# Performance work log

Hardware: AMD Instinct MI355X
Metric: run time of the kernel (lower is better)

The kernel has to match this reference:

```python
import jax, jax.numpy as jnp
import numpy as np

TP, M, K, N_GLOBAL = 8, 4096, 8192, 8192
K_LOCAL = K // TP      # 1024
N_LOCAL = N_GLOBAL // TP  # 1024


def setup_inputs() -> dict:
    key = jax.random.key(0)
    k1, k2, k3 = jax.random.split(key, 3)
    # all_act[r] is rank r's local activation shard (M, K_local);
    # the fused kernel all-gathers these into the gathered buffer.
    all_act = jax.random.normal(k1, (TP, M, K_LOCAL), dtype=jnp.float32)
    # local_W: this rank's weight shard, full K rows, N_local columns.
    local_W = jax.random.normal(k2, (K, N_LOCAL), dtype=jnp.float32) / np.sqrt(K)
    bias = jax.random.normal(k3, (N_LOCAL,), dtype=jnp.float32)
    return {"all_act": all_act, "local_W": local_W, "bias": bias}


def reference(all_act, local_W, bias):
    # Kernel accumulates, per source rank r:
    #   acc += A_shard[r] (M, K_local) @ W[r*K_local:(r+1)*K_local] (K_local, N_local)
    # which equals A_full @ W_local with A_full the K-concat of shards.
    W_shards = local_W.reshape(TP, K_LOCAL, N_LOCAL)
    out = jnp.einsum('rmk,rkn->mn', all_act, W_shards)  # (M, N_local)
    return out + bias[None, :]
```

## Files before the change

kernel.cpp:

```cpp
#include <hip/hip_runtime.h>
#include <stdint.h>

#define TP_      8
#define M_DIM    4096
#define K_DIM    8192
#define N_DIM    1024
#define KL_      1024
#define BM       256
#define BN       256
#define SPLITK   4
#define KSLICE   (K_DIM / SPLITK)
#define MN4      (M_DIM * N_DIM / 4)
#define KCHUNKS  (K_DIM / 32)
#define NBLK_A   ((M_DIM / 16) * (K_DIM / 32) / 4)
#define NBLK_W   ((N_DIM / 64) * (K_DIM / 64))

typedef _Float16 f16;
typedef f16 f16x8 __attribute__((ext_vector_type(8)));
typedef f16 f16x4 __attribute__((ext_vector_type(4)));
typedef float f32x4 __attribute__((ext_vector_type(4)));

__device__ __forceinline__ f16x8 cvt8(float4 a, float4 b) {
    f16x8 r;
    r[0] = (f16)a.x; r[1] = (f16)a.y; r[2] = (f16)a.z; r[3] = (f16)a.w;
    r[4] = (f16)b.x; r[5] = (f16)b.y; r[6] = (f16)b.z; r[7] = (f16)b.w;
    return r;
}

__device__ __forceinline__ void lds_load16(const void* g, void* l) {
    __builtin_amdgcn_global_load_lds(
        (const __attribute__((address_space(1))) void*)g,
        (__attribute__((address_space(3))) void*)l, 16, 0, 0);
}


__global__ __launch_bounds__(256) void conv_aw_kernel(
        const float* __restrict__ act, const float* __restrict__ W,
        f16* __restrict__ Afrag, f16* __restrict__ Bfrag) {
    __shared__ float tile[64][68];
    const int bid = blockIdx.x;
    const int t   = threadIdx.x;
    if (bid < NBLK_A) {
        const int chunkId = bid * 4 + (t >> 6);
        const int lane = t & 63;
        const int q  = lane >> 4;
        const int rr = lane & 15;
        const int mg  = chunkId >> 8;
        const int k32 = chunkId & 255;
        const int k  = k32 * 32 + q * 8;
        const int r  = k >> 10;
        const int kl = k & (KL_ - 1);
        const int m  = mg * 16 + rr;
        const float4* src = (const float4*)(act + ((size_t)r * M_DIM + m) * KL_ + kl);
        float4 a = src[0], b = src[1];
        *(f16x8*)(Afrag + (size_t)chunkId * 512 + lane * 8) = cvt8(a, b);
        return;
    }
    const int b2 = bid - NBLK_A;
    const int n0 = (b2 & 15) * 64;
    const int k0 = (b2 >> 4) * 64;
    #pragma unroll
    for (int l = 0; l < 4; l++) {
        int kr = l * 16 + (t >> 4);
        float4 v = *(const float4*)&W[(size_t)(k0 + kr) * N_DIM + n0 + (t & 15) * 4];
        *(float4*)&tile[kr][(t & 15) * 4] = v;
    }
    __syncthreads();
    const int jtl   = t >> 6;
    const int kt32l = (t >> 5) & 1;
    const int u     = t & 31;
    const int rr    = u & 15;
    const int qp    = u >> 4;
    f16x8 h0, h1;
    #pragma unroll
    for (int kk = 0; kk < 8; kk++)
        h0[kk] = (f16)tile[kt32l * 32 + qp * 16 + kk][jtl * 16 + rr];
    #pragma unroll
    for (int kk = 0; kk < 8; kk++)
        h1[kk] = (f16)tile[kt32l * 32 + qp * 16 + 8 + kk][jtl * 16 + rr];
    size_t chunk = (size_t)(n0 / 16 + jtl) * KCHUNKS + (k0 / 32 + kt32l);
    f16* dst = Bfrag + chunk * 512;
    *(f16x8*)(dst + ((2 * qp)     * 16 + rr) * 8) = h0;
    *(f16x8*)(dst + ((2 * qp + 1) * 16 + rr) * 8) = h1;
}

__global__ __launch_bounds__(512, 2) void gemm_frag_kernel(
        const f16* __restrict__ Afrag,
        const f16* __restrict__ Bfrag,
        f16* __restrict__ part) {
    __shared__ f16 sm[2][64 * 512];

    const int tid  = threadIdx.x;
    const int w    = tid >> 6;
    const int lane = tid & 63;
    const int q    = lane >> 4;
    const int rr   = lane & 15;
    const int wr   = w >> 2;
    const int wc   = w & 3;

    const int id   = blockIdx.x;
    const int xcd  = id & 7;
    const int slot = id >> 3;
    const int z    = xcd >> 1;
    const int mb   = (slot >> 2) * 2 + (xcd & 1);
    const int nb   = slot & 3;
    const int row0 = mb * BM;
    const int col0 = nb * BN;
    const int kb32 = z * (KSLICE / 32);
    const int mg0  = row0 >> 4;
    const int ng0  = col0 >> 4;

    f32x4 acc[8][4];
    #pragma unroll
    for (int m = 0; m < 8; m++)
        #pragma unroll
        for (int n = 0; n < 4; n++)
            acc[m][n] = (f32x4){0.f, 0.f, 0.f, 0.f};

    f16x8 af[8];
    f16x8 bf[2];

#define STAGE_A(B_, T_, K2_) do { \
    const int kt32_ = kb32 + 2 * (T_) + (K2_); \
    _Pragma("unroll") \
    for (int j_ = 0; j_ < 2; j_++) { \
        const int mg_ = 2 * w + j_; \
        const f16* g_ = Afrag + ((size_t)(mg0 + mg_) * KCHUNKS + kt32_) * 512 + lane * 8; \
        lds_load16(g_, &sm[B_][(mg_ * 2 + (K2_)) * 512 + lane * 8]); \
    } \
} while (0)

#define STAGE_B(B_, T_, K2_) do { \
    const int kt32_ = kb32 + 2 * (T_) + (K2_); \
    _Pragma("unroll") \
    for (int j_ = 0; j_ < 2; j_++) { \
        const int ng_ = 2 * w + j_; \
        const f16* g_ = Bfrag + ((size_t)(ng0 + ng_) * KCHUNKS + kt32_) * 512 + lane * 8; \
        lds_load16(g_, &sm[B_][(32 + ng_ * 2 + (K2_)) * 512 + lane * 8]); \
    } \
} while (0)

#define READ_A(B_, K2_) do { \
    _Pragma("unroll") \
    for (int mi_ = 0; mi_ < 8; mi_++) \
        af[mi_] = *(const f16x8*)&sm[B_][((wr * 8 + mi_) * 2 + (K2_)) * 512 + lane * 8]; \
} while (0)

#define READ_B(B_, K2_, NH_) do { \
    _Pragma("unroll") \
    for (int ni_ = 0; ni_ < 2; ni_++) \
        bf[ni_] = *(const f16x8*)&sm[B_][(32 + (wc * 4 + (NH_) * 2 + ni_) * 2 + (K2_)) * 512 + lane * 8]; \
} while (0)

#define MFMA16(NH_) do { \
    __builtin_amdgcn_s_setprio(1); \
    _Pragma("unroll") \
    for (int mi_ = 0; mi_ < 8; mi_++) \
        _Pragma("unroll") \
        for (int ni_ = 0; ni_ < 2; ni_++) \
            acc[mi_][(NH_) * 2 + ni_] = __builtin_amdgcn_mfma_f32_16x16x32_f16( \
                af[mi_], bf[ni_], acc[mi_][(NH_) * 2 + ni_], 0, 0, 0); \
    __builtin_amdgcn_s_setprio(0); \
} while (0)

#define BAR() do { \
    asm volatile("" ::: "memory"); \
    __builtin_amdgcn_s_barrier(); \
    asm volatile("" ::: "memory"); \
} while (0)
#define SBAR0() __builtin_amdgcn_sched_barrier(0)
#define VM4() asm volatile("s_waitcnt vmcnt(4)" ::: "memory")
#define VM0() asm volatile("s_waitcnt vmcnt(0)" ::: "memory")

#define TILE(P_, T_, STG_, VMMID_, VMEND_) do { \
    READ_A(P_, 0); READ_B(P_, 0, 0); \
    if (STG_) STAGE_A((P_) ^ 1, (T_) + 1, 0); \
    BAR(); SBAR0(); MFMA16(0); BAR(); \
    READ_B(P_, 0, 1); \
    if (STG_) STAGE_B((P_) ^ 1, (T_) + 1, 0); \
    BAR(); SBAR0(); MFMA16(1); VMMID_; BAR(); \
    READ_A(P_, 1); READ_B(P_, 1, 0); \
    if (STG_) STAGE_A((P_) ^ 1, (T_) + 1, 1); \
    BAR(); SBAR0(); MFMA16(0); BAR(); \
    READ_B(P_, 1, 1); \
    if (STG_) STAGE_B((P_) ^ 1, (T_) + 1, 1); \
    BAR(); SBAR0(); MFMA16(1); VMEND_; BAR(); \
} while (0)

    STAGE_A(0, 0, 0);
    STAGE_B(0, 0, 0);
    STAGE_A(0, 0, 1);
    STAGE_B(0, 0, 1);
    VM4();
    BAR();

    #pragma unroll 1
    for (int t = 0; t < 30; t += 2) {
        TILE(0, t,     1, VM4(), VM4());
        TILE(1, t + 1, 1, VM4(), VM4());
    }
    TILE(0, 30, 1, VM4(), VM4());
    TILE(1, 31, 0, VM0(), (void)0);

    f16* Pz = part + (size_t)z * M_DIM * N_DIM;
    #pragma unroll
    for (int m = 0; m < 8; m++) {
        const int gm = row0 + wr * 128 + m * 16 + q * 4;
        #pragma unroll
        for (int n = 0; n < 4; n++) {
            const int gn = col0 + wc * 64 + n * 16 + rr;
            #pragma unroll
            for (int r2 = 0; r2 < 4; r2++)
                Pz[(size_t)(gm + r2) * N_DIM + gn] = (f16)acc[m][n][r2];
        }
    }
#undef STAGE_A
#undef STAGE_B
#undef READ_A
#undef READ_B
#undef MFMA16
#undef BAR
#undef SBAR0
#undef VM4
#undef VM0
#undef TILE
}

__global__ __launch_bounds__(256) void reduce_kernel(
        const f16* __restrict__ part, const float* __restrict__ bias,
        float* __restrict__ out) {
    int p = blockIdx.x * 256 + threadIdx.x;
    const f16x4* P = (const f16x4*)part;
    f16x4 s0 = P[p];
    f16x4 s1 = P[p + MN4];
    f16x4 s2 = P[p + 2 * MN4];
    f16x4 s3 = P[p + 3 * MN4];
    float4 b  = ((const float4*)bias)[p & (N_DIM / 4 - 1)];
    float4 r;
    r.x = (float)s0[0] + (float)s1[0] + (float)s2[0] + (float)s3[0] + b.x;
    r.y = (float)s0[1] + (float)s1[1] + (float)s2[1] + (float)s3[1] + b.y;
    r.z = (float)s0[2] + (float)s1[2] + (float)s2[2] + (float)s3[2] + b.z;
    r.w = (float)s0[3] + (float)s1[3] + (float)s2[3] + (float)s3[3] + b.w;
    ((float4*)out)[p] = r;
}

__global__ void gemm_fallback_kernel(const float* __restrict__ act,
                                     const float* __restrict__ W,
                                     const float* __restrict__ bias,
                                     float* __restrict__ out) {
    __shared__ float sA2[32][33];
    __shared__ float sB2[32][33];
    int tx = threadIdx.x, ty = threadIdx.y;
    int m = blockIdx.y * 32 + ty;
    int n = blockIdx.x * 32 + tx;
    float acc = 0.f;
    for (int kt = 0; kt < K_DIM; kt += 32) {
        int ka = kt + tx;
        int r = ka >> 10, kl = ka & (KL_ - 1);
        sA2[ty][tx] = act[((size_t)r * M_DIM + m) * KL_ + kl];
        sB2[ty][tx] = W[(size_t)(kt + ty) * N_DIM + n];
        __syncthreads();
        #pragma unroll
        for (int kk = 0; kk < 32; kk++) acc += sA2[ty][kk] * sB2[kk][tx];
        __syncthreads();
    }
    out[(size_t)m * N_DIM + n] = acc + bias[n];
}

extern "C" void kernel_launch(void* const* d_in, const int* in_sizes, int n_in,
                              void* d_out, int out_size, void* d_ws, size_t ws_size,
                              hipStream_t stream) {
    const float* all_act = (const float*)d_in[0];
    const float* local_W = (const float*)d_in[1];
    const float* bias    = (const float*)d_in[2];
    float* out = (float*)d_out;

    const size_t partBytes = (size_t)SPLITK * M_DIM * N_DIM * sizeof(f16);
    const size_t elemsA    = (size_t)M_DIM * K_DIM;
    const size_t elemsW    = (size_t)K_DIM * N_DIM;
    const size_t need = partBytes + elemsA * sizeof(f16) + elemsW * sizeof(f16);

    if (ws_size < need) {
        gemm_fallback_kernel<<<dim3(N_DIM / 32, M_DIM / 32), dim3(32, 32), 0, stream>>>(
            all_act, local_W, bias, out);
        return;
    }

    f16* part  = (f16*)d_ws;
    f16* Afrag = (f16*)((char*)d_ws + partBytes);
    f16* Bfrag = Afrag + elemsA;

    conv_aw_kernel<<<NBLK_A + NBLK_W, 256, 0, stream>>>(all_act, local_W, Afrag, Bfrag);
    gemm_frag_kernel<<<256, 512, 0, stream>>>(Afrag, Bfrag, part);
    reduce_kernel<<<MN4 / 256, 256, 0, stream>>>(part, bias, out);
}
```

Before: 294.7 us.

## Fuse activation fp32-to-fp16 conversion into GEMM via swizzled LDS staging

Drops the separate pass that converted activations to fp16 fragment layout. The GEMM now loads fp32 activations straight into LDS through a swizzled layout and converts them to fp16 while reading fragments. Tile shape changes to BM=128 with split-K of 2, so the reduce kernel sums two partials instead of four. This removes a 128MB-scale read/write round trip of the activation buffer. In exchange the GEMM moves twice as many A bytes, uses 128KB of LDS per block, and spends extra VALU work on conversion inside the main loop.

Result: slower. 363.4 us (+23.3%).

```diff
diff --git a/kernel.cpp b/kernel.cpp
--- a/kernel.cpp
+++ b/kernel.cpp
@@ -6,14 +6,13 @@
 #define K_DIM    8192
 #define N_DIM    1024
 #define KL_      1024
-#define BM       256
+#define BM       128
 #define BN       256
-#define SPLITK   4
+#define SPLITK   2
 #define KSLICE   (K_DIM / SPLITK)
+#define NT       (KSLICE / 64)
 #define MN4      (M_DIM * N_DIM / 4)
 #define KCHUNKS  (K_DIM / 32)
-#define NBLK_A   ((M_DIM / 16) * (K_DIM / 32) / 4)
-#define NBLK_W   ((N_DIM / 64) * (K_DIM / 64))
 
 typedef _Float16 f16;
 typedef f16 f16x8 __attribute__((ext_vector_type(8)));
@@ -33,32 +32,12 @@
         (__attribute__((address_space(3))) void*)l, 16, 0, 0);
 }
 
-
-__global__ __launch_bounds__(256) void conv_aw_kernel(
-        const float* __restrict__ act, const float* __restrict__ W,
-        f16* __restrict__ Afrag, f16* __restrict__ Bfrag) {
+__global__ __launch_bounds__(256) void conv_w_kernel(
+        const float* __restrict__ W, f16* __restrict__ Bfrag) {
     __shared__ float tile[64][68];
-    const int bid = blockIdx.x;
-    const int t   = threadIdx.x;
-    if (bid < NBLK_A) {
-        const int chunkId = bid * 4 + (t >> 6);
-        const int lane = t & 63;
-        const int q  = lane >> 4;
-        const int rr = lane & 15;
-        const int mg  = chunkId >> 8;
-        const int k32 = chunkId & 255;
-        const int k  = k32 * 32 + q * 8;
-        const int r  = k >> 10;
-        const int kl = k & (KL_ - 1);
-        const int m  = mg * 16 + rr;
-        const float4* src = (const float4*)(act + ((size_t)r * M_DIM + m) * KL_ + kl);
-        float4 a = src[0], b = src[1];
-        *(f16x8*)(Afrag + (size_t)chunkId * 512 + lane * 8) = cvt8(a, b);
-        return;
-    }
-    const int b2 = bid - NBLK_A;
-    const int n0 = (b2 & 15) * 64;
-    const int k0 = (b2 >> 4) * 64;
+    const int t  = threadIdx.x;
+    const int n0 = blockIdx.x * 64;
+    const int k0 = blockIdx.y * 64;
     #pragma unroll
     for (int l = 0; l < 4; l++) {
         int kr = l * 16 + (t >> 4);
@@ -84,11 +63,13 @@
     *(f16x8*)(dst + ((2 * qp + 1) * 16 + rr) * 8) = h1;
 }
 
-__global__ __launch_bounds__(512, 2) void gemm_frag_kernel(
-        const f16* __restrict__ Afrag,
+__global__ __launch_bounds__(512, 2) void gemm_fused_kernel(
+        const float* __restrict__ act,
         const f16* __restrict__ Bfrag,
         f16* __restrict__ part) {
-    __shared__ f16 sm[2][64 * 512];
+    __shared__ __align__(16) char smraw[131072];
+    char* const smA = smraw;
+    char* const smB = smraw + 65536;
 
     const int tid  = threadIdx.x;
     const int w    = tid >> 6;
@@ -101,32 +82,38 @@
     const int id   = blockIdx.x;
     const int xcd  = id & 7;
     const int slot = id >> 3;
-    const int z    = xcd >> 1;
-    const int mb   = (slot >> 2) * 2 + (xcd & 1);
+    const int z    = xcd & 1;
+    const int mgrp = xcd >> 1;
+    const int mb   = (slot >> 2) * 4 + mgrp;
     const int nb   = slot & 3;
     const int row0 = mb * BM;
     const int col0 = nb * BN;
     const int kb32 = z * (KSLICE / 32);
-    const int mg0  = row0 >> 4;
     const int ng0  = col0 >> 4;
 
-    f32x4 acc[8][4];
-    #pragma unroll
-    for (int m = 0; m < 8; m++)
+    const int aColX  = (((lane & 7) ^ (lane >> 3)) << 2);
+    const int aRowIn = lane >> 3;
+    const int aOff0  = rr * 128 + ((((2 * q)) ^ (rr & 7)) << 4);
+
+    f32x4 acc[4][4];
+    #pragma unroll
+    for (int m = 0; m < 4; m++)
         #pragma unroll
         for (int n = 0; n < 4; n++)
             acc[m][n] = (f32x4){0.f, 0.f, 0.f, 0.f};
 
-    f16x8 af[8];
-    f16x8 bf[2];
+    f16x8 af[4];
+    f16x8 bf[4];
 
 #define STAGE_A(B_, T_, K2_) do { \
     const int kt32_ = kb32 + 2 * (T_) + (K2_); \
+    const int r_  = kt32_ >> 5; \
+    const int kl_ = (kt32_ & 31) * 32; \
     _Pragma("unroll") \
     for (int j_ = 0; j_ < 2; j_++) { \
-        const int mg_ = 2 * w + j_; \
-        const f16* g_ = Afrag + ((size_t)(mg0 + mg_) * KCHUNKS + kt32_) * 512 + lane * 8; \
-        lds_load16(g_, &sm[B_][(mg_ * 2 + (K2_)) * 512 + lane * 8]); \
+        const float* g_ = act + ((size_t)r_ * M_DIM + row0 + w * 16 + j_ * 8 + aRowIn) * KL_ \
+                          + kl_ + aColX; \
+        lds_load16(g_, smA + (((B_) * 2 + (K2_)) * 8 + w) * 2048 + j_ * 1024 + lane * 16); \
     } \
 } while (0)
 
@@ -136,30 +123,34 @@
     for (int j_ = 0; j_ < 2; j_++) { \
         const int ng_ = 2 * w + j_; \
         const f16* g_ = Bfrag + ((size_t)(ng0 + ng_) * KCHUNKS + kt32_) * 512 + lane * 8; \
-        lds_load16(g_, &sm[B_][(32 + ng_ * 2 + (K2_)) * 512 + lane * 8]); \
+        lds_load16(g_, smB + (((B_) * 2 + (K2_)) * 16 + ng_) * 1024 + lane * 16); \
     } \
 } while (0)
 
 #define READ_A(B_, K2_) do { \
     _Pragma("unroll") \
-    for (int mi_ = 0; mi_ < 8; mi_++) \
-        af[mi_] = *(const f16x8*)&sm[B_][((wr * 8 + mi_) * 2 + (K2_)) * 512 + lane * 8]; \
-} while (0)
-
-#define READ_B(B_, K2_, NH_) do { \
-    _Pragma("unroll") \
-    for (int ni_ = 0; ni_ < 2; ni_++) \
-        bf[ni_] = *(const f16x8*)&sm[B_][(32 + (wc * 4 + (NH_) * 2 + ni_) * 2 + (K2_)) * 512 + lane * 8]; \
-} while (0)
-
-#define MFMA16(NH_) do { \
+    for (int mi_ = 0; mi_ < 4; mi_++) { \
+        const char* b_ = smA + (((B_) * 2 + (K2_)) * 8 + wr * 4 + mi_) * 2048 + aOff0; \
+        float4 x_ = *(const float4*)(b_); \
+        float4 y_ = *(const float4*)(b_ + ((aOff0 ^ 16) - aOff0)); \
+        af[mi_] = cvt8(x_, y_); \
+    } \
+} while (0)
+
+#define READ_B(B_, K2_) do { \
+    _Pragma("unroll") \
+    for (int ni_ = 0; ni_ < 4; ni_++) \
+        bf[ni_] = *(const f16x8*)(smB + (((B_) * 2 + (K2_)) * 16 + wc * 4 + ni_) * 1024 + lane * 16); \
+} while (0)
+
+#define MFMA16() do { \
     __builtin_amdgcn_s_setprio(1); \
     _Pragma("unroll") \
-    for (int mi_ = 0; mi_ < 8; mi_++) \
+    for (int mi_ = 0; mi_ < 4; mi_++) \
         _Pragma("unroll") \
-        for (int ni_ = 0; ni_ < 2; ni_++) \
-            acc[mi_][(NH_) * 2 + ni_] = __builtin_amdgcn_mfma_f32_16x16x32_f16( \
-                af[mi_], bf[ni_], acc[mi_][(NH_) * 2 + ni_], 0, 0, 0); \
+        for (int ni_ = 0; ni_ < 4; ni_++) \
+            acc[mi_][ni_] = __builtin_amdgcn_mfma_f32_16x16x32_f16( \
+                af[mi_], bf[ni_], acc[mi_][ni_], 0, 0, 0); \
     __builtin_amdgcn_s_setprio(0); \
 } while (0)
 
@@ -173,18 +164,12 @@
 #define VM0() asm volatile("s_waitcnt vmcnt(0)" ::: "memory")
 
 #define TILE(P_, T_, STG_, VMMID_, VMEND_) do { \
-    READ_A(P_, 0); READ_B(P_, 0, 0); \
-    if (STG_) STAGE_A((P_) ^ 1, (T_) + 1, 0); \
-    BAR(); SBAR0(); MFMA16(0); BAR(); \
-    READ_B(P_, 0, 1); \
-    if (STG_) STAGE_B((P_) ^ 1, (T_) + 1, 0); \
-    BAR(); SBAR0(); MFMA16(1); VMMID_; BAR(); \
-    READ_A(P_, 1); READ_B(P_, 1, 0); \
-    if (STG_) STAGE_A((P_) ^ 1, (T_) + 1, 1); \
-    BAR(); SBAR0(); MFMA16(0); BAR(); \
-    READ_B(P_, 1, 1); \
-    if (STG_) STAGE_B((P_) ^ 1, (T_) + 1, 1); \
-    BAR(); SBAR0(); MFMA16(1); VMEND_; BAR(); \
+    READ_A(P_, 0); READ_B(P_, 0); \
+    if (STG_) { STAGE_A((P_) ^ 1, (T_) + 1, 0); STAGE_B((P_) ^ 1, (T_) + 1, 0); } \
+    BAR(); SBAR0(); MFMA16(); VMMID_; BAR(); \
+    READ_A(P_, 1); READ_B(P_, 1); \
+    if (STG_) { STAGE_A((P_) ^ 1, (T_) + 1, 1); STAGE_B((P_) ^ 1, (T_) + 1, 1); } \
+    BAR(); SBAR0(); MFMA16(); VMEND_; BAR(); \
 } while (0)
 
     STAGE_A(0, 0, 0);
@@ -195,17 +180,17 @@
     BAR();
 
     #pragma unroll 1
-    for (int t = 0; t < 30; t += 2) {
+    for (int t = 0; t < 62; t += 2) {
         TILE(0, t,     1, VM4(), VM4());
         TILE(1, t + 1, 1, VM4(), VM4());
     }
-    TILE(0, 30, 1, VM4(), VM4());
-    TILE(1, 31, 0, VM0(), (void)0);
+    TILE(0, 62, 1, VM4(), VM4());
+    TILE(1, 63, 0, VM0(), (void)0);
 
     f16* Pz = part + (size_t)z * M_DIM * N_DIM;
     #pragma unroll
-    for (int m = 0; m < 8; m++) {
-        const int gm = row0 + wr * 128 + m * 16 + q * 4;
+    for (int m = 0; m < 4; m++) {
+        const int gm = row0 + wr * 64 + m * 16 + q * 4;
         #pragma unroll
         for (int n = 0; n < 4; n++) {
             const int gn = col0 + wc * 64 + n * 16 + rr;
@@ -233,14 +218,12 @@
     const f16x4* P = (const f16x4*)part;
     f16x4 s0 = P[p];
     f16x4 s1 = P[p + MN4];
-    f16x4 s2 = P[p + 2 * MN4];
-    f16x4 s3 = P[p + 3 * MN4];
     float4 b  = ((const float4*)bias)[p & (N_DIM / 4 - 1)];
     float4 r;
-    r.x = (float)s0[0] + (float)s1[0] + (float)s2[0] + (float)s3[0] + b.x;
-    r.y = (float)s0[1] + (float)s1[1] + (float)s2[1] + (float)s3[1] + b.y;
-    r.z = (float)s0[2] + (float)s1[2] + (float)s2[2] + (float)s3[2] + b.z;
-    r.w = (float)s0[3] + (float)s1[3] + (float)s2[3] + (float)s3[3] + b.w;
+    r.x = (float)s0[0] + (float)s1[0] + b.x;
+    r.y = (float)s0[1] + (float)s1[1] + b.y;
+    r.z = (float)s0[2] + (float)s1[2] + b.z;
+    r.w = (float)s0[3] + (float)s1[3] + b.w;
     ((float4*)out)[p] = r;
 }
 
@@ -276,9 +259,8 @@
     float* out = (float*)d_out;
 
     const size_t partBytes = (size_t)SPLITK * M_DIM * N_DIM * sizeof(f16);
-    const size_t elemsA    = (size_t)M_DIM * K_DIM;
     const size_t elemsW    = (size_t)K_DIM * N_DIM;
-    const size_t need = partBytes + elemsA * sizeof(f16) + elemsW * sizeof(f16);
+    const size_t need = partBytes + elemsW * sizeof(f16);
 
     if (ws_size < need) {
         gemm_fallback_kernel<<<dim3(N_DIM / 32, M_DIM / 32), dim3(32, 32), 0, stream>>>(
@@ -287,10 +269,9 @@
     }
 
     f16* part  = (f16*)d_ws;
-    f16* Afrag = (f16*)((char*)d_ws + partBytes);
-    f16* Bfrag = Afrag + elemsA;
-
-    conv_aw_kernel<<<NBLK_A + NBLK_W, 256, 0, stream>>>(all_act, local_W, Afrag, Bfrag);
-    gemm_frag_kernel<<<256, 512, 0, stream>>>(Afrag, Bfrag, part);
+    f16* Bfrag = (f16*)((char*)d_ws + partBytes);
+
+    conv_w_kernel<<<dim3(N_DIM / 64, K_DIM / 64), 256, 0, stream>>>(local_W, Bfrag);
+    gemm_fused_kernel<<<256, 512, 0, stream>>>(all_act, Bfrag, part);
     reduce_kernel<<<MN4 / 256, 256, 0, stream>>>(part, bias, out);
 }
```
